# Kernel tuning notes

Hardware: AMD Instinct MI355X
Metric: run time of the kernel (lower is better)

## Reference

```python
import jax, jax.numpy as jnp
import numpy as np
import math

D_MODEL = 768
NUM_HEADS = 12
D_K = D_MODEL // NUM_HEADS
B, S = 4, 2048


def setup_inputs() -> dict:
    key = jax.random.key(0)
    ks = jax.random.split(key, 11)
    s = 1.0 / math.sqrt(D_MODEL)
    inp = {
        "q": jax.random.normal(ks[0], (B, S, D_MODEL), jnp.float32),
        "k": jax.random.normal(ks[1], (B, S, D_MODEL), jnp.float32),
        "v": jax.random.normal(ks[2], (B, S, D_MODEL), jnp.float32),
        "w_q": jax.random.normal(ks[3], (D_MODEL, D_MODEL), jnp.float32) * s,
        "b_q": jax.random.normal(ks[4], (D_MODEL,), jnp.float32) * s,
        "w_k": jax.random.normal(ks[5], (D_MODEL, D_MODEL), jnp.float32) * s,
        "b_k": jax.random.normal(ks[6], (D_MODEL,), jnp.float32) * s,
        "w_v": jax.random.normal(ks[7], (D_MODEL, D_MODEL), jnp.float32) * s,
        "b_v": jax.random.normal(ks[8], (D_MODEL,), jnp.float32) * s,
        "w_o": jax.random.normal(ks[9], (D_MODEL, D_MODEL), jnp.float32) * s,
        "b_o": jax.random.normal(ks[10], (D_MODEL,), jnp.float32) * s,
    }
    return inp


def reference(q, k, v, w_q, b_q, w_k, b_k, w_v, b_v, w_o, b_o):
    b = q.shape[0]
    # Linear projections (torch Linear: x @ W.T + b), reshape to [B,H,S,d_k]
    def proj(x, w, bias):
        y = x @ w.T + bias
        return y.reshape(b, -1, NUM_HEADS, D_K).transpose(0, 2, 1, 3)

    qh = proj(q, w_q, b_q)
    kh = proj(k, w_k, b_k)
    vh = proj(v, w_v, b_v)

    scale = 1.0 / math.sqrt(D_K)
    scores = jnp.einsum("bhqd,bhkd->bhqk", qh, kh) * scale  # [B,H,S,S]
    attn = jax.nn.softmax(scores, axis=-1)
    # dropout is identity in eval mode
    out = jnp.einsum("bhqk,bhkd->bhqd", attn, vh)
    out = out.transpose(0, 2, 1, 3).reshape(b, -1, D_MODEL)
    return out @ w_o.T + b_o
```

## Files before the change

### kernel.cpp

```cpp
#include <hip/hip_runtime.h>

#define DEV __device__ __forceinline__

typedef __attribute__((ext_vector_type(8))) short short8;
typedef __attribute__((ext_vector_type(4))) float f32x4;
typedef unsigned short u16;
typedef unsigned int u32;

DEV f32x4 mfma16(short8 a, short8 b, f32x4 c) {
    return __builtin_amdgcn_mfma_f32_16x16x32_bf16(a, b, c, 0, 0, 0);
}

DEV u16 f2bf(float f) {
    unsigned u = __builtin_bit_cast(unsigned, f);
    u += 0x7fffu + ((u >> 16) & 1u);
    return (u16)(u >> 16);
}

DEV u32 cvt_pk_bf16(float a, float b) {
    u32 r;
    asm("v_cvt_pk_bf16_f32 %0, %1, %2" : "=v"(r) : "v"(a), "v"(b));
    return r;
}

DEV float fexp2_scaled(float xs) {
    int i = (int)xs + 1065055420;
    return __builtin_bit_cast(float, i);
}

DEV void gload16(const void* g, const void* l) {
    __builtin_amdgcn_global_load_lds(
        (const __attribute__((address_space(1))) unsigned int*)g,
        (__attribute__((address_space(3))) unsigned int*)l, 16, 0, 0);
}

template<int N> DEV void waitvm_barrier() {
    asm volatile("s_waitcnt vmcnt(%0)\n\ts_barrier" :: "n"(N) : "memory");
}

DEV short8 lds_frag_swz(const u16* base, int row, int chunk) {
    int sc = chunk ^ (row & 7);
    return *(const short8*)((const char*)base + row * 128 + sc * 16);
}

__global__ __launch_bounds__(256) void prep(
    const float* __restrict__ q, const float* __restrict__ k, const float* __restrict__ v,
    const float* __restrict__ wq, const float* __restrict__ wk,
    const float* __restrict__ wv, const float* __restrict__ wo,
    u16* __restrict__ xq, u16* __restrict__ xk, u16* __restrict__ xv,
    u16* __restrict__ wqB, u16* __restrict__ wkB, u16* __restrict__ wvB,
    u16* __restrict__ woB)
{
    int b = blockIdx.x;
    const float* s;
    u16* d;
    int i;
    if (b < 18432) {
        int t = b / 6144, r = b % 6144;
        s = t == 0 ? q : t == 1 ? k : v;
        d = t == 0 ? xq : t == 1 ? xk : xv;
        i = r * 256 + threadIdx.x;
    } else {
        int t = (b - 18432) / 576, r = (b - 18432) % 576;
        s = t == 0 ? wq : t == 1 ? wk : t == 2 ? wv : wo;
        d = t == 0 ? wqB : t == 1 ? wkB : t == 2 ? wvB : woB;
        i = r * 256 + threadIdx.x;
    }
    float4 vv = ((const float4*)s)[i];
    ((ushort4*)d)[i] = make_ushort4(f2bf(vv.x), f2bf(vv.y), f2bf(vv.z), f2bf(vv.w));
}

template<int MODE>
DEV void gemm_bf16_body(const u16* __restrict__ A_g, const u16* __restrict__ B_g,
                        const float* __restrict__ bias, float scale,
                        u16* __restrict__ outP, float* __restrict__ outF,
                        int mBase, int nBase)
{
    __shared__ u16 AS[128 * 64], BS[128 * 64];

    const int tid = threadIdx.x;
    const int l = tid & 63, wid = tid >> 6;
    const int wy = wid >> 1, wx = wid & 1;
    const int lr = l & 15, lg = l >> 4;

    f32x4 acc[4][4];
    for (int i = 0; i < 4; ++i)
        for (int j = 0; j < 4; ++j) acc[i][j] = (f32x4)0.0f;

    for (int kt = 0; kt < 12; ++kt) {
        if (kt) __syncthreads();
        for (int r = 0; r < 4; ++r) {
            int c = tid + r * 256;
            int row = c >> 3;
            int sc = (c & 7) ^ (row & 7);
            size_t gA = (size_t)(mBase + row) * 768 + kt * 64 + sc * 8;
            size_t gB = (size_t)(nBase + row) * 768 + kt * 64 + sc * 8;
            gload16(A_g + gA, AS + (size_t)(r * 256 + wid * 64) * 8);
            gload16(B_g + gB, BS + (size_t)(r * 256 + wid * 64) * 8);
        }
        __syncthreads();

        short8 bf[4][2];
        for (int nt = 0; nt < 4; ++nt)
            for (int ks = 0; ks < 2; ++ks)
                bf[nt][ks] = lds_frag_swz(BS, wx * 64 + nt * 16 + lr, ks * 4 + lg);
        for (int mt = 0; mt < 4; ++mt) {
            short8 ah[2];
            for (int ks = 0; ks < 2; ++ks)
                ah[ks] = lds_frag_swz(AS, wy * 64 + mt * 16 + lr, ks * 4 + lg);
            for (int nt = 0; nt < 4; ++nt)
                for (int ks = 0; ks < 2; ++ks)
                    acc[mt][nt] = mfma16(ah[ks], bf[nt][ks], acc[mt][nt]);
        }
    }

    for (int mt = 0; mt < 4; ++mt)
        for (int nt = 0; nt < 4; ++nt) {
            int colg = nBase + wx * 64 + nt * 16 + lr;
            for (int r = 0; r < 4; ++r) {
                int rowg = mBase + wy * 64 + mt * 16 + lg * 4 + r;
                float bv = (MODE == 2) ? bias[rowg] : bias[colg];
                float vv = (acc[mt][nt][r] + bv) * scale;
                if constexpr (MODE == 0) {
                    int b = rowg >> 11, s = rowg & 2047;
                    int h = colg >> 6, d = colg & 63;
                    outP[((size_t)(b * 12 + h) * 2048 + s) * 64 + d] = f2bf(vv);
                } else if constexpr (MODE == 1) {
                    outF[(size_t)rowg * 768 + colg] = vv;
                } else {
                    int b = colg >> 11, s = colg & 2047;
                    int h = rowg >> 6, d = rowg & 63;
                    outP[((size_t)(b * 12 + h) * 64 + d) * 2048 + s] = f2bf(vv);
                }
            }
        }
}

__global__ __launch_bounds__(256, 4) void gemm_proj(
    const u16* __restrict__ xq, const u16* __restrict__ xk, const u16* __restrict__ xv,
    const u16* __restrict__ wq, const u16* __restrict__ wk, const u16* __restrict__ wv,
    const float* __restrict__ bq, const float* __restrict__ bk, const float* __restrict__ bv,
    u16* __restrict__ Qpl, u16* __restrict__ Kpl, u16* __restrict__ Vtp)
{
    int z = blockIdx.z;
    if (z < 2) {
        const u16* X = z ? xk : xq;
        const u16* W = z ? wk : wq;
        const float* bias = z ? bk : bq;
        float scale = z ? 1.0f : 0.125f * 1.44269504f * 8388608.0f;
        u16* o = z ? Kpl : Qpl;
        gemm_bf16_body<0>(X, W, bias, scale, o, nullptr, blockIdx.y * 128, blockIdx.x * 128);
    } else {
        gemm_bf16_body<2>(wv, xv, bv, 1.0f, Vtp, nullptr, blockIdx.x * 128, blockIdx.y * 128);
    }
}

__global__ __launch_bounds__(256, 4) void gemm_out(
    const u16* __restrict__ Op, const u16* __restrict__ woB,
    const float* __restrict__ bias, float* __restrict__ outF)
{
    gemm_bf16_body<1>(Op, woB, bias, 1.0f, nullptr, outF,
                      blockIdx.y * 128, blockIdx.x * 128);
}

__global__ __launch_bounds__(256, 3) void attn4(
    const u16* __restrict__ Qp, const u16* __restrict__ Kp,
    const u16* __restrict__ Vtp, u16* __restrict__ Op)
{
    __shared__ u16 Ks[2][64 * 64], Vs[2][64 * 64];
    __shared__ u16 Eh[128][72];

    const int tid = threadIdx.x;
    const int l = tid & 63, wid = tid >> 6;
    const int lr = l & 15, lg = l >> 4;
    const int bh = blockIdx.x, qt = blockIdx.y;

    short8 q_h[2][2];
    for (int s = 0; s < 2; ++s) {
        size_t qrow = ((size_t)bh * 2048 + qt * 128 + wid * 32 + s * 16 + lr) * 64;
        q_h[s][0] = *(const short8*)(Qp + qrow + lg * 8);
        q_h[s][1] = *(const short8*)(Qp + qrow + 32 + lg * 8);
    }

    short8 ones;
    for (int j = 0; j < 8; ++j) ones[j] = (short)0x3F80;

    f32x4 num[2][4];
    for (int s = 0; s < 2; ++s)
        for (int nt = 0; nt < 4; ++nt) num[s][nt] = (f32x4)0.0f;
    f32x4 denacc[2] = {(f32x4)0.0f, (f32x4)0.0f};

    auto stageK = [&](int kb, int p) {
        for (int r = 0; r < 2; ++r) {
            int c = tid + r * 256;
            int row = c >> 3, sc = (c & 7) ^ (row & 7);
            size_t g = ((size_t)bh * 2048 + kb * 64 + row) * 64 + sc * 8;
            gload16(Kp + g, Ks[p] + (size_t)(r * 256 + wid * 64) * 8);
        }
    };
    auto stageV = [&](int kb, int p) {
        for (int r = 0; r < 2; ++r) {
            int c = tid + r * 256;
            int row = c >> 3, sc = (c & 7) ^ (row & 7);
            size_t g = ((size_t)bh * 64 + row) * 2048 + kb * 64 + sc * 8;
            gload16(Vtp + g, Vs[p] + (size_t)(r * 256 + wid * 64) * 8);
        }
    };

    stageK(0, 0);
    stageV(0, 0);

    for (int kb = 0; kb < 32; ++kb) {
        const int p = kb & 1;
        waitvm_barrier<0>();
        if (kb < 31) {
            stageK(kb + 1, p ^ 1);
            stageV(kb + 1, p ^ 1);
        }

        f32x4 st[2][4];
        for (int s = 0; s < 2; ++s)
            for (int nt = 0; nt < 4; ++nt) st[s][nt] = (f32x4)0.0f;
        __builtin_amdgcn_s_setprio(1);
        for (int nt = 0; nt < 4; ++nt)
            for (int ks = 0; ks < 2; ++ks) {
                short8 kh = lds_frag_swz(Ks[p], nt * 16 + lr, ks * 4 + lg);
                st[0][nt] = mfma16(kh, q_h[0][ks], st[0][nt]);
                st[1][nt] = mfma16(kh, q_h[1][ks], st[1][nt]);
            }
        __builtin_amdgcn_s_setprio(0);

        for (int s = 0; s < 2; ++s)
            for (int nt = 0; nt < 4; ++nt) {
                u32 pk0 = cvt_pk_bf16(fexp2_scaled(st[s][nt][0]), fexp2_scaled(st[s][nt][1]));
                u32 pk1 = cvt_pk_bf16(fexp2_scaled(st[s][nt][2]), fexp2_scaled(st[s][nt][3]));
                int erow = wid * 32 + s * 16 + lr;
                *(u32*)&Eh[erow][nt * 16 + lg * 4]     = pk0;
                *(u32*)&Eh[erow][nt * 16 + lg * 4 + 2] = pk1;
            }

        short8 e[2][2];
        for (int s = 0; s < 2; ++s) {
            int erow = wid * 32 + s * 16 + lr;
            e[s][0] = *(const short8*)&Eh[erow][lg * 8];
            e[s][1] = *(const short8*)&Eh[erow][32 + lg * 8];
        }
        __builtin_amdgcn_s_setprio(1);
        denacc[0] = mfma16(e[0][0], ones, denacc[0]);
        denacc[0] = mfma16(e[0][1], ones, denacc[0]);
        denacc[1] = mfma16(e[1][0], ones, denacc[1]);
        denacc[1] = mfma16(e[1][1], ones, denacc[1]);
        for (int nt = 0; nt < 4; ++nt)
            for (int ks = 0; ks < 2; ++ks) {
                short8 vh = lds_frag_swz(Vs[p], nt * 16 + lr, ks * 4 + lg);
                num[0][nt] = mfma16(e[0][ks], vh, num[0][nt]);
                num[1][nt] = mfma16(e[1][ks], vh, num[1][nt]);
            }
        __builtin_amdgcn_s_setprio(0);
    }

    const int b = bh / 12, h = bh % 12;
    for (int s = 0; s < 2; ++s) {
        float rden[4];
        for (int r = 0; r < 4; ++r) rden[r] = 1.0f / denacc[s][r];
        for (int nt = 0; nt < 4; ++nt)
            for (int r = 0; r < 4; ++r) {
                int srow = qt * 128 + wid * 32 + s * 16 + lg * 4 + r;
                size_t rowg = (size_t)b * 2048 + srow;
                int col = h * 64 + nt * 16 + lr;
                Op[rowg * 768 + col] = f2bf(num[s][nt][r] * rden[r]);
            }
    }
}

extern "C" void kernel_launch(void* const* d_in, const int* in_sizes, int n_in,
                              void* d_out, int out_size, void* d_ws, size_t ws_size,
                              hipStream_t stream)
{
    const float* q   = (const float*)d_in[0];
    const float* k   = (const float*)d_in[1];
    const float* v   = (const float*)d_in[2];
    const float* w_q = (const float*)d_in[3];
    const float* b_q = (const float*)d_in[4];
    const float* w_k = (const float*)d_in[5];
    const float* b_k = (const float*)d_in[6];
    const float* w_v = (const float*)d_in[7];
    const float* b_v = (const float*)d_in[8];
    const float* w_o = (const float*)d_in[9];
    const float* b_o = (const float*)d_in[10];
    float* out = (float*)d_out;

    const size_t PL  = (size_t)48 * 2048 * 64;
    const size_t WPL = (size_t)768 * 768;
    u16* base = (u16*)d_ws;
    u16* xqB = base;
    u16* xkB = base + PL;
    u16* xvB = base + 2 * PL;
    u16* Qpl = base + 3 * PL;
    u16* Kpl = base + 4 * PL;
    u16* Vtp = base + 5 * PL;
    u16* OP  = base + 6 * PL;
    u16* W   = base + 7 * PL;
    u16* wqB = W;
    u16* wkB = W + WPL;
    u16* wvB = W + 2 * WPL;
    u16* woB = W + 3 * WPL;

    dim3 bt(256, 1, 1);
    hipLaunchKernelGGL(prep, dim3(20736), bt, 0, stream,
                       q, k, v, w_q, w_k, w_v, w_o,
                       xqB, xkB, xvB, wqB, wkB, wvB, woB);

    hipLaunchKernelGGL(gemm_proj, dim3(6, 64, 3), bt, 0, stream,
                       xqB, xkB, xvB, wqB, wkB, wvB, b_q, b_k, b_v,
                       Qpl, Kpl, Vtp);

    hipLaunchKernelGGL(attn4, dim3(48, 16), bt, 0, stream,
                       Qpl, Kpl, Vtp, OP);

    hipLaunchKernelGGL(gemm_out, dim3(6, 64), bt, 0, stream,
                       OP, woB, b_o, out);
}
```

Before: 156.0 us.

## Restructure attention to two waves with 64 query rows each and swizzled P tile

The attention kernel now uses 128 threads (two waves) per block, each wave handling 64 query rows instead of 32. This doubles the reuse of every K/V LDS fragment read per MFMA and halves the number of waves sharing each staged tile. The padded E (probability) buffer is replaced by an XOR-swizzled layout read through the same fragment helper, avoiding padding and bank conflicts. The cost is higher register pressure (more accumulators) and fewer waves to hide latency. The projection GEMM dispatch is also split into explicit branches.

```diff
diff --git a/kernel.cpp b/kernel.cpp
--- a/kernel.cpp
+++ b/kernel.cpp
@@ -71,10 +71,10 @@
 }
 
 template<int MODE>
-DEV void gemm_bf16_body(const u16* __restrict__ A_g, const u16* __restrict__ B_g,
-                        const float* __restrict__ bias, float scale,
-                        u16* __restrict__ outP, float* __restrict__ outF,
-                        int mBase, int nBase)
+DEV void gemm_body(const u16* __restrict__ A_g, const u16* __restrict__ B_g,
+                   const float* __restrict__ bias, float scale,
+                   u16* __restrict__ outP, float* __restrict__ outF,
+                   int mBase, int nBase)
 {
     __shared__ u16 AS[128 * 64], BS[128 * 64];
 
@@ -138,20 +138,20 @@
 
 __global__ __launch_bounds__(256, 4) void gemm_proj(
     const u16* __restrict__ xq, const u16* __restrict__ xk, const u16* __restrict__ xv,
-    const u16* __restrict__ wq, const u16* __restrict__ wk, const u16* __restrict__ wv,
+    const u16* __restrict__ wqB, const u16* __restrict__ wkB, const u16* __restrict__ wvB,
     const float* __restrict__ bq, const float* __restrict__ bk, const float* __restrict__ bv,
     u16* __restrict__ Qpl, u16* __restrict__ Kpl, u16* __restrict__ Vtp)
 {
     int z = blockIdx.z;
-    if (z < 2) {
-        const u16* X = z ? xk : xq;
-        const u16* W = z ? wk : wq;
-        const float* bias = z ? bk : bq;
-        float scale = z ? 1.0f : 0.125f * 1.44269504f * 8388608.0f;
-        u16* o = z ? Kpl : Qpl;
-        gemm_bf16_body<0>(X, W, bias, scale, o, nullptr, blockIdx.y * 128, blockIdx.x * 128);
+    if (z == 0) {
+        gemm_body<0>(xq, wqB, bq, 0.125f * 1.44269504f * 8388608.0f, Qpl, nullptr,
+                     blockIdx.y * 128, blockIdx.x * 128);
+    } else if (z == 1) {
+        gemm_body<0>(xk, wkB, bk, 1.0f, Kpl, nullptr,
+                     blockIdx.y * 128, blockIdx.x * 128);
     } else {
-        gemm_bf16_body<2>(wv, xv, bv, 1.0f, Vtp, nullptr, blockIdx.x * 128, blockIdx.y * 128);
+        gemm_body<2>(wvB, xv, bv, 1.0f, Vtp, nullptr,
+                     blockIdx.x * 128, blockIdx.y * 128);
     }
 }
 
@@ -159,25 +159,25 @@
     const u16* __restrict__ Op, const u16* __restrict__ woB,
     const float* __restrict__ bias, float* __restrict__ outF)
 {
-    gemm_bf16_body<1>(Op, woB, bias, 1.0f, nullptr, outF,
-                      blockIdx.y * 128, blockIdx.x * 128);
-}
-
-__global__ __launch_bounds__(256, 3) void attn4(
+    gemm_body<1>(Op, woB, bias, 1.0f, nullptr, outF,
+                 blockIdx.y * 128, blockIdx.x * 128);
+}
+
+__global__ __launch_bounds__(128, 2) void attn2(
     const u16* __restrict__ Qp, const u16* __restrict__ Kp,
     const u16* __restrict__ Vtp, u16* __restrict__ Op)
 {
     __shared__ u16 Ks[2][64 * 64], Vs[2][64 * 64];
-    __shared__ u16 Eh[128][72];
+    __shared__ u16 Eh[128 * 64];
 
     const int tid = threadIdx.x;
     const int l = tid & 63, wid = tid >> 6;
     const int lr = l & 15, lg = l >> 4;
     const int bh = blockIdx.x, qt = blockIdx.y;
 
-    short8 q_h[2][2];
-    for (int s = 0; s < 2; ++s) {
-        size_t qrow = ((size_t)bh * 2048 + qt * 128 + wid * 32 + s * 16 + lr) * 64;
+    short8 q_h[4][2];
+    for (int s = 0; s < 4; ++s) {
+        size_t qrow = ((size_t)bh * 2048 + qt * 128 + wid * 64 + s * 16 + lr) * 64;
         q_h[s][0] = *(const short8*)(Qp + qrow + lg * 8);
         q_h[s][1] = *(const short8*)(Qp + qrow + 32 + lg * 8);
     }
@@ -185,25 +185,26 @@
     short8 ones;
     for (int j = 0; j < 8; ++j) ones[j] = (short)0x3F80;
 
-    f32x4 num[2][4];
-    for (int s = 0; s < 2; ++s)
+    f32x4 num[4][4];
+    for (int s = 0; s < 4; ++s)
         for (int nt = 0; nt < 4; ++nt) num[s][nt] = (f32x4)0.0f;
-    f32x4 denacc[2] = {(f32x4)0.0f, (f32x4)0.0f};
+    f32x4 denacc[4];
+    for (int s = 0; s < 4; ++s) denacc[s] = (f32x4)0.0f;
 
     auto stageK = [&](int kb, int p) {
-        for (int r = 0; r < 2; ++r) {
-            int c = tid + r * 256;
+        for (int r = 0; r < 4; ++r) {
+            int c = r * 128 + tid;
             int row = c >> 3, sc = (c & 7) ^ (row & 7);
             size_t g = ((size_t)bh * 2048 + kb * 64 + row) * 64 + sc * 8;
-            gload16(Kp + g, Ks[p] + (size_t)(r * 256 + wid * 64) * 8);
+            gload16(Kp + g, Ks[p] + (size_t)(r * 128 + wid * 64) * 8);
         }
     };
     auto stageV = [&](int kb, int p) {
-        for (int r = 0; r < 2; ++r) {
-            int c = tid + r * 256;
+        for (int r = 0; r < 4; ++r) {
+            int c = r * 128 + tid;
             int row = c >> 3, sc = (c & 7) ^ (row & 7);
             size_t g = ((size_t)bh * 64 + row) * 2048 + kb * 64 + sc * 8;
-            gload16(Vtp + g, Vs[p] + (size_t)(r * 256 + wid * 64) * 8);
+            gload16(Vtp + g, Vs[p] + (size_t)(r * 128 + wid * 64) * 8);
         }
     };
 
@@ -218,8 +219,8 @@
             stageV(kb + 1, p ^ 1);
         }
 
-        f32x4 st[2][4];
-        for (int s = 0; s < 2; ++s)
+        f32x4 st[4][4];
+        for (int s = 0; s < 4; ++s)
             for (int nt = 0; nt < 4; ++nt) st[s][nt] = (f32x4)0.0f;
         __builtin_amdgcn_s_setprio(1);
         for (int nt = 0; nt < 4; ++nt)
@@ -227,45 +228,48 @@
                 short8 kh = lds_frag_swz(Ks[p], nt * 16 + lr, ks * 4 + lg);
                 st[0][nt] = mfma16(kh, q_h[0][ks], st[0][nt]);
                 st[1][nt] = mfma16(kh, q_h[1][ks], st[1][nt]);
+                st[2][nt] = mfma16(kh, q_h[2][ks], st[2][nt]);
+                st[3][nt] = mfma16(kh, q_h[3][ks], st[3][nt]);
             }
         __builtin_amdgcn_s_setprio(0);
 
-        for (int s = 0; s < 2; ++s)
+        for (int s = 0; s < 4; ++s)
             for (int nt = 0; nt < 4; ++nt) {
                 u32 pk0 = cvt_pk_bf16(fexp2_scaled(st[s][nt][0]), fexp2_scaled(st[s][nt][1]));
                 u32 pk1 = cvt_pk_bf16(fexp2_scaled(st[s][nt][2]), fexp2_scaled(st[s][nt][3]));
-                int erow = wid * 32 + s * 16 + lr;
-                *(u32*)&Eh[erow][nt * 16 + lg * 4]     = pk0;
-                *(u32*)&Eh[erow][nt * 16 + lg * 4 + 2] = pk1;
-            }
-
-        short8 e[2][2];
-        for (int s = 0; s < 2; ++s) {
-            int erow = wid * 32 + s * 16 + lr;
-            e[s][0] = *(const short8*)&Eh[erow][lg * 8];
-            e[s][1] = *(const short8*)&Eh[erow][32 + lg * 8];
-        }
+                int row = wid * 64 + s * 16 + lr;
+                int chunk = (2 * nt + (lg >> 1)) ^ (row & 7);
+                char* pb = (char*)Eh + row * 128 + chunk * 16 + (lg & 1) * 8;
+                *(uint2*)pb = make_uint2(pk0, pk1);
+            }
+
+        short8 e[4][2];
+        for (int s = 0; s < 4; ++s)
+            for (int ks = 0; ks < 2; ++ks)
+                e[s][ks] = lds_frag_swz(Eh, wid * 64 + s * 16 + lr, ks * 4 + lg);
         __builtin_amdgcn_s_setprio(1);
-        denacc[0] = mfma16(e[0][0], ones, denacc[0]);
-        denacc[0] = mfma16(e[0][1], ones, denacc[0]);
-        denacc[1] = mfma16(e[1][0], ones, denacc[1]);
-        denacc[1] = mfma16(e[1][1], ones, denacc[1]);
+        for (int s = 0; s < 4; ++s) {
+            denacc[s] = mfma16(e[s][0], ones, denacc[s]);
+            denacc[s] = mfma16(e[s][1], ones, denacc[s]);
+        }
         for (int nt = 0; nt < 4; ++nt)
             for (int ks = 0; ks < 2; ++ks) {
                 short8 vh = lds_frag_swz(Vs[p], nt * 16 + lr, ks * 4 + lg);
                 num[0][nt] = mfma16(e[0][ks], vh, num[0][nt]);
                 num[1][nt] = mfma16(e[1][ks], vh, num[1][nt]);
+                num[2][nt] = mfma16(e[2][ks], vh, num[2][nt]);
+                num[3][nt] = mfma16(e[3][ks], vh, num[3][nt]);
             }
         __builtin_amdgcn_s_setprio(0);
     }
 
     const int b = bh / 12, h = bh % 12;
-    for (int s = 0; s < 2; ++s) {
+    for (int s = 0; s < 4; ++s) {
         float rden[4];
         for (int r = 0; r < 4; ++r) rden[r] = 1.0f / denacc[s][r];
         for (int nt = 0; nt < 4; ++nt)
             for (int r = 0; r < 4; ++r) {
-                int srow = qt * 128 + wid * 32 + s * 16 + lg * 4 + r;
+                int srow = qt * 128 + wid * 64 + s * 16 + lg * 4 + r;
                 size_t rowg = (size_t)b * 2048 + srow;
                 int col = h * 64 + nt * 16 + lr;
                 Op[rowg * 768 + col] = f2bf(num[s][nt][r] * rden[r]);
@@ -315,7 +319,7 @@
                        xqB, xkB, xvB, wqB, wkB, wvB, b_q, b_k, b_v,
                        Qpl, Kpl, Vtp);
 
-    hipLaunchKernelGGL(attn4, dim3(48, 16), bt, 0, stream,
+    hipLaunchKernelGGL(attn2, dim3(48, 16), dim3(128, 1, 1), 0, stream,
                        Qpl, Kpl, Vtp, OP);
 
     hipLaunchKernelGGL(gemm_out, dim3(6, 64), bt, 0, stream,
```

Result: slower. 165.0 us (+5.8%).

## Shrink GEMM M-tile to 64, swizzle attention E buffer, raise attn occupancy

Applied to the files above, without the earlier changes.

The projection and output GEMMs now use 64x128 tiles instead of 128x128, doubling the grid so more workgroups fill the CUs. The V projection remaps block ids to cover the transposed 768x8192 shape. In attention, the padded E staging buffer becomes an XOR-swizzled 128x64 layout, which shrinks LDS so launch bounds can request 4 waves-per-EU occupancy. The smaller tiles lower operand reuse per workgroup and add more global loads in exchange for better parallelism.

```diff
diff --git a/kernel.cpp b/kernel.cpp
--- a/kernel.cpp
+++ b/kernel.cpp
@@ -71,31 +71,36 @@
 }
 
 template<int MODE>
-DEV void gemm_bf16_body(const u16* __restrict__ A_g, const u16* __restrict__ B_g,
-                        const float* __restrict__ bias, float scale,
-                        u16* __restrict__ outP, float* __restrict__ outF,
-                        int mBase, int nBase)
-{
-    __shared__ u16 AS[128 * 64], BS[128 * 64];
+DEV void gemm_body(const u16* __restrict__ A_g, const u16* __restrict__ B_g,
+                   const float* __restrict__ bias, float scale,
+                   u16* __restrict__ outP, float* __restrict__ outF,
+                   int mBase, int nBase)
+{
+    __shared__ u16 AS[64 * 64], BS[128 * 64];
 
     const int tid = threadIdx.x;
     const int l = tid & 63, wid = tid >> 6;
     const int wy = wid >> 1, wx = wid & 1;
     const int lr = l & 15, lg = l >> 4;
 
-    f32x4 acc[4][4];
-    for (int i = 0; i < 4; ++i)
+    f32x4 acc[2][4];
+    for (int i = 0; i < 2; ++i)
         for (int j = 0; j < 4; ++j) acc[i][j] = (f32x4)0.0f;
 
     for (int kt = 0; kt < 12; ++kt) {
         if (kt) __syncthreads();
+        for (int r = 0; r < 2; ++r) {
+            int c = tid + r * 256;
+            int row = c >> 3;
+            int sc = (c & 7) ^ (row & 7);
+            size_t gA = (size_t)(mBase + row) * 768 + kt * 64 + sc * 8;
+            gload16(A_g + gA, AS + (size_t)(r * 256 + wid * 64) * 8);
+        }
         for (int r = 0; r < 4; ++r) {
             int c = tid + r * 256;
             int row = c >> 3;
             int sc = (c & 7) ^ (row & 7);
-            size_t gA = (size_t)(mBase + row) * 768 + kt * 64 + sc * 8;
             size_t gB = (size_t)(nBase + row) * 768 + kt * 64 + sc * 8;
-            gload16(A_g + gA, AS + (size_t)(r * 256 + wid * 64) * 8);
             gload16(B_g + gB, BS + (size_t)(r * 256 + wid * 64) * 8);
         }
         __syncthreads();
@@ -104,21 +109,21 @@
         for (int nt = 0; nt < 4; ++nt)
             for (int ks = 0; ks < 2; ++ks)
                 bf[nt][ks] = lds_frag_swz(BS, wx * 64 + nt * 16 + lr, ks * 4 + lg);
-        for (int mt = 0; mt < 4; ++mt) {
+        for (int mt = 0; mt < 2; ++mt) {
             short8 ah[2];
             for (int ks = 0; ks < 2; ++ks)
-                ah[ks] = lds_frag_swz(AS, wy * 64 + mt * 16 + lr, ks * 4 + lg);
+                ah[ks] = lds_frag_swz(AS, wy * 32 + mt * 16 + lr, ks * 4 + lg);
             for (int nt = 0; nt < 4; ++nt)
                 for (int ks = 0; ks < 2; ++ks)
                     acc[mt][nt] = mfma16(ah[ks], bf[nt][ks], acc[mt][nt]);
         }
     }
 
-    for (int mt = 0; mt < 4; ++mt)
+    for (int mt = 0; mt < 2; ++mt)
         for (int nt = 0; nt < 4; ++nt) {
             int colg = nBase + wx * 64 + nt * 16 + lr;
             for (int r = 0; r < 4; ++r) {
-                int rowg = mBase + wy * 64 + mt * 16 + lg * 4 + r;
+                int rowg = mBase + wy * 32 + mt * 16 + lg * 4 + r;
                 float bv = (MODE == 2) ? bias[rowg] : bias[colg];
                 float vv = (acc[mt][nt][r] + bv) * scale;
                 if constexpr (MODE == 0) {
@@ -138,20 +143,21 @@
 
 __global__ __launch_bounds__(256, 4) void gemm_proj(
     const u16* __restrict__ xq, const u16* __restrict__ xk, const u16* __restrict__ xv,
-    const u16* __restrict__ wq, const u16* __restrict__ wk, const u16* __restrict__ wv,
+    const u16* __restrict__ wqB, const u16* __restrict__ wkB, const u16* __restrict__ wvB,
     const float* __restrict__ bq, const float* __restrict__ bk, const float* __restrict__ bv,
     u16* __restrict__ Qpl, u16* __restrict__ Kpl, u16* __restrict__ Vtp)
 {
     int z = blockIdx.z;
-    if (z < 2) {
-        const u16* X = z ? xk : xq;
-        const u16* W = z ? wk : wq;
-        const float* bias = z ? bk : bq;
-        float scale = z ? 1.0f : 0.125f * 1.44269504f * 8388608.0f;
-        u16* o = z ? Kpl : Qpl;
-        gemm_bf16_body<0>(X, W, bias, scale, o, nullptr, blockIdx.y * 128, blockIdx.x * 128);
+    if (z == 0) {
+        gemm_body<0>(xq, wqB, bq, 0.125f * 1.44269504f * 8388608.0f, Qpl, nullptr,
+                     blockIdx.y * 64, blockIdx.x * 128);
+    } else if (z == 1) {
+        gemm_body<0>(xk, wkB, bk, 1.0f, Kpl, nullptr,
+                     blockIdx.y * 64, blockIdx.x * 128);
     } else {
-        gemm_bf16_body<2>(wv, xv, bv, 1.0f, Vtp, nullptr, blockIdx.x * 128, blockIdx.y * 128);
+        int id = blockIdx.y * 6 + blockIdx.x;
+        gemm_body<2>(wvB, xv, bv, 1.0f, Vtp, nullptr,
+                     (id % 12) * 64, (id / 12) * 128);
     }
 }
 
@@ -159,16 +165,16 @@
     const u16* __restrict__ Op, const u16* __restrict__ woB,
     const float* __restrict__ bias, float* __restrict__ outF)
 {
-    gemm_bf16_body<1>(Op, woB, bias, 1.0f, nullptr, outF,
-                      blockIdx.y * 128, blockIdx.x * 128);
-}
-
-__global__ __launch_bounds__(256, 3) void attn4(
+    gemm_body<1>(Op, woB, bias, 1.0f, nullptr, outF,
+                 blockIdx.y * 64, blockIdx.x * 128);
+}
+
+__global__ __launch_bounds__(256, 4) void attn4(
     const u16* __restrict__ Qp, const u16* __restrict__ Kp,
     const u16* __restrict__ Vtp, u16* __restrict__ Op)
 {
     __shared__ u16 Ks[2][64 * 64], Vs[2][64 * 64];
-    __shared__ u16 Eh[128][72];
+    __shared__ u16 Eh[128 * 64];
 
     const int tid = threadIdx.x;
     const int l = tid & 63, wid = tid >> 6;
@@ -234,22 +240,21 @@
             for (int nt = 0; nt < 4; ++nt) {
                 u32 pk0 = cvt_pk_bf16(fexp2_scaled(st[s][nt][0]), fexp2_scaled(st[s][nt][1]));
                 u32 pk1 = cvt_pk_bf16(fexp2_scaled(st[s][nt][2]), fexp2_scaled(st[s][nt][3]));
-                int erow = wid * 32 + s * 16 + lr;
-                *(u32*)&Eh[erow][nt * 16 + lg * 4]     = pk0;
-                *(u32*)&Eh[erow][nt * 16 + lg * 4 + 2] = pk1;
+                int row = wid * 32 + s * 16 + lr;
+                int chunk = (2 * nt + (lg >> 1)) ^ (row & 7);
+                char* pb = (char*)Eh + row * 128 + chunk * 16 + (lg & 1) * 8;
+                *(uint2*)pb = make_uint2(pk0, pk1);
             }
 
         short8 e[2][2];
+        for (int s = 0; s < 2; ++s)
+            for (int ks = 0; ks < 2; ++ks)
+                e[s][ks] = lds_frag_swz(Eh, wid * 32 + s * 16 + lr, ks * 4 + lg);
+        __builtin_amdgcn_s_setprio(1);
         for (int s = 0; s < 2; ++s) {
-            int erow = wid * 32 + s * 16 + lr;
-            e[s][0] = *(const short8*)&Eh[erow][lg * 8];
-            e[s][1] = *(const short8*)&Eh[erow][32 + lg * 8];
-        }
-        __builtin_amdgcn_s_setprio(1);
-        denacc[0] = mfma16(e[0][0], ones, denacc[0]);
-        denacc[0] = mfma16(e[0][1], ones, denacc[0]);
-        denacc[1] = mfma16(e[1][0], ones, denacc[1]);
-        denacc[1] = mfma16(e[1][1], ones, denacc[1]);
+            denacc[s] = mfma16(e[s][0], ones, denacc[s]);
+            denacc[s] = mfma16(e[s][1], ones, denacc[s]);
+        }
         for (int nt = 0; nt < 4; ++nt)
             for (int ks = 0; ks < 2; ++ks) {
                 short8 vh = lds_frag_swz(Vs[p], nt * 16 + lr, ks * 4 + lg);
@@ -311,13 +316,13 @@
                        q, k, v, w_q, w_k, w_v, w_o,
                        xqB, xkB, xvB, wqB, wkB, wvB, woB);
 
-    hipLaunchKernelGGL(gemm_proj, dim3(6, 64, 3), bt, 0, stream,
+    hipLaunchKernelGGL(gemm_proj, dim3(6, 128, 3), bt, 0, stream,
                        xqB, xkB, xvB, wqB, wkB, wvB, b_q, b_k, b_v,
                        Qpl, Kpl, Vtp);
 
     hipLaunchKernelGGL(attn4, dim3(48, 16), bt, 0, stream,
                        Qpl, Kpl, Vtp, OP);
 
-    hipLaunchKernelGGL(gemm_out, dim3(6, 64), bt, 0, stream,
+    hipLaunchKernelGGL(gemm_out, dim3(6, 128), bt, 0, stream,
                        OP, woB, b_o, out);
 }
```

Result: slower. 161.8 us (+3.8%).
